# Optimization experiments

Measured on AMD Instinct MI355X. Metric: run time of the kernel, lower is better.

## Reference

```python
import jax, jax.numpy as jnp
import numpy as np

MASK_ID = 3
MAX_SEN = 128
SEN_DIM = 128
EMBED = 1024


def setup_inputs() -> dict:
    key = jax.random.key(0)
    ks = jax.random.split(key, 12)
    B, S, E, D = 8, 8192, EMBED, SEN_DIM
    s = 0.02
    return {
        "input_ids": jax.random.randint(ks[0], (B, S), 0, 64),
        "hidden_states": jax.random.normal(ks[1], (B, S, E), jnp.float32),
        "Wv": jax.random.normal(ks[2], (E, D), jnp.float32) * s,
        "bv": jnp.zeros((D,), jnp.float32),
        "Wq": jax.random.normal(ks[3], (E, D), jnp.float32) * s,
        "bq": jnp.zeros((D,), jnp.float32),
        "Wk": jax.random.normal(ks[4], (D, D), jnp.float32) * s,
        "bk": jnp.zeros((D,), jnp.float32),
        "Wvt": jax.random.normal(ks[5], (D, D), jnp.float32) * s,
        "bvt": jnp.zeros((D,), jnp.float32),
        "Wo": jax.random.normal(ks[6], (D, E), jnp.float32) * s,
        "bo": jnp.zeros((E,), jnp.float32),
    }


def reference(input_ids, hidden_states, Wv, bv, Wq, bq, Wk, bk, Wvt, bvt, Wo, bo):
    B, S, E = hidden_states.shape
    dt = hidden_states.dtype

    # sentence segmentation: each mask token t with running count c belongs to bucket c-1
    mask = input_ids == MASK_ID                               # (B, S)
    csum = jnp.cumsum(mask.astype(jnp.int32), axis=1)         # (B, S)
    # tokens that are not mask tokens (or overflow max_sen_num) go to dummy bucket MAX_SEN
    seg = jnp.where(mask & (csum <= MAX_SEN), csum - 1, MAX_SEN)  # (B, S)

    # segment-sum replacement for torch.bmm(sen_pos_mask, hidden_states)
    b_idx = jnp.arange(B)[:, None]
    pooled = jnp.zeros((B, MAX_SEN + 1, E), dt).at[b_idx, seg].add(hidden_states)[:, :MAX_SEN]  # (B, M, E)

    static_sen_states = pooled @ Wv + bv                      # (B, M, 128)

    q_token = (hidden_states @ Wq + bq) * (SEN_DIM ** -0.5)   # (B, S, 128)
    k_sen = static_sen_states @ Wk + bk                       # (B, M, 128)
    v_sen = static_sen_states @ Wvt + bvt                     # (B, M, 128)

    # token t may attend to sentences 0..csum[t]-1
    tmp_mask = (jnp.arange(MAX_SEN)[None, None, :] + 1) <= csum[:, :, None]  # (B, S, M)
    neg = jnp.finfo(dt).min
    logits = jnp.einsum('bsd,bmd->bsm', q_token, k_sen) + jnp.where(tmp_mask, jnp.zeros((), dt), neg)
    attn = jax.nn.softmax(logits, axis=-1) * tmp_mask.astype(dt)  # (B, S, M)

    sen_attn_output = jnp.einsum('bsm,bmd->bsd', attn, v_sen) @ Wo + bo  # (B, S, E)
    return sen_attn_output
```

## Files before the change

kernel.cpp:

```cpp
#include <hip/hip_runtime.h>
#include <hip/hip_bf16.h>

#define MASK_ID 3
#define MAX_SEN 128
#define NB 8
#define SEQ 8192
#define EMB 1024
#define DIM 128

typedef __attribute__((ext_vector_type(8))) short short8v;
typedef __attribute__((ext_vector_type(4))) float f32x4;

#define MFMA(a, b, c) __builtin_amdgcn_mfma_f32_16x16x32_bf16(a, b, c, 0, 0, 0)

__device__ __forceinline__ short f2b(float x) {
    union { float f; unsigned u; } v; v.f = x;
    unsigned r = (v.u + 0x7FFFu + ((v.u >> 16) & 1u)) >> 16;
    return (short)r;
}

__device__ __forceinline__ unsigned cvtpk(float a, float b) {
    unsigned r;
    asm("v_cvt_pk_bf16_f32 %0, %1, %2" : "=v"(r) : "v"(a), "v"(b));
    return r;
}

__global__ __launch_bounds__(1024) void seg_kernel(const int* __restrict__ ids,
                                                   int* __restrict__ pos,
                                                   int* __restrict__ nvis) {
    int b = blockIdx.x;
    int tid = threadIdx.x;
    __shared__ int sc[1024];
    __shared__ int sc2[1024];
    const int PER = SEQ / 1024;
    int base = b * SEQ + tid * PER;

    int ids_l[PER];
    int cnt = 0;
    #pragma unroll
    for (int j = 0; j < PER; j++) {
        ids_l[j] = ids[base + j];
        cnt += (ids_l[j] == MASK_ID) ? 1 : 0;
    }
    if (tid < MAX_SEN) pos[b * MAX_SEN + tid] = -1;
    sc[tid] = cnt;
    __syncthreads();

    int* src = sc;
    int* dst = sc2;
    for (int off = 1; off < 1024; off <<= 1) {
        int v = src[tid];
        if (tid >= off) v += src[tid - off];
        dst[tid] = v;
        __syncthreads();
        int* t = src; src = dst; dst = t;
    }
    int incl = src[tid];
    int run = incl - cnt;

    #pragma unroll
    for (int j = 0; j < PER; j++) {
        if (ids_l[j] == MASK_ID) {
            run++;
            if (run <= MAX_SEN) pos[b * MAX_SEN + run - 1] = tid * PER + j;
        }
        int nv = run; if (nv > MAX_SEN) nv = MAX_SEN;
        nvis[base + j] = nv;
    }
}

__global__ __launch_bounds__(256) void prep_w(const float* __restrict__ Wq,
                                              const float* __restrict__ Wo,
                                              short* __restrict__ WqTt,
                                              short* __restrict__ WoTt) {
    int t = blockIdx.x * 256 + threadIdx.x;
    {
        int fid = t >> 6, lp = t & 63;
        int c = fid >> 4, ks = (fid >> 3) & 1, cf = fid & 7;
        int e0 = c * 64 + ks * 32 + (lp >> 4) * 8;
        int d = cf * 16 + (lp & 15);
        short8v v;
        #pragma unroll
        for (int j = 0; j < 8; j++) v[j] = f2b(Wq[(size_t)(e0 + j) * 128 + d]);
        *(short8v*)(WqTt + fid * 512 + lp * 8) = v;
    }
    {
        int fid = t >> 6, lp = t & 63;
        int ef = fid >> 2, kk = fid & 3;
        int e = ef * 16 + (lp & 15);
        int dd0 = kk * 32 + (lp >> 4) * 8;
        short8v v;
        #pragma unroll
        for (int j = 0; j < 8; j++) v[j] = f2b(Wo[(size_t)(dd0 + j) * 1024 + e]);
        *(short8v*)(WoTt + fid * 512 + lp * 8) = v;
    }
}

__global__ __launch_bounds__(128) void statkv_kernel(const float* __restrict__ hidden,
                                                     const float* __restrict__ Wv, const float* __restrict__ bv,
                                                     const float* __restrict__ Wk, const float* __restrict__ bk,
                                                     const float* __restrict__ Wvt, const float* __restrict__ bvt,
                                                     const int* __restrict__ pos,
                                                     short* __restrict__ k_t, short* __restrict__ vT_t) {
    int mg = blockIdx.x;
    int b  = blockIdx.y;
    int d  = threadIdx.x;
    __shared__ float h[4][1024];
    __shared__ float st[4][128];
    int m0 = mg * 4;

    #pragma unroll
    for (int j = 0; j < 4; j++) {
        int p = pos[b * MAX_SEN + m0 + j];
        const float* hp = hidden + ((size_t)b * SEQ + (p < 0 ? 0 : p)) * EMB;
        #pragma unroll
        for (int ii = 0; ii < 2; ii++) {
            float4 v = {0.f, 0.f, 0.f, 0.f};
            if (p >= 0) v = *(const float4*)(hp + ii * 512 + d * 4);
            *(float4*)&h[j][ii * 512 + d * 4] = v;
        }
    }
    __syncthreads();

    float a0 = 0.f, a1 = 0.f, a2 = 0.f, a3 = 0.f;
    for (int e = 0; e < 1024; e += 4) {
        float w0 = Wv[(size_t)e * 128 + d];
        float w1 = Wv[(size_t)(e + 1) * 128 + d];
        float w2 = Wv[(size_t)(e + 2) * 128 + d];
        float w3 = Wv[(size_t)(e + 3) * 128 + d];
        float4 h0 = *(const float4*)&h[0][e];
        float4 h1 = *(const float4*)&h[1][e];
        float4 h2 = *(const float4*)&h[2][e];
        float4 h3 = *(const float4*)&h[3][e];
        a0 += h0.x * w0 + h0.y * w1 + h0.z * w2 + h0.w * w3;
        a1 += h1.x * w0 + h1.y * w1 + h1.z * w2 + h1.w * w3;
        a2 += h2.x * w0 + h2.y * w1 + h2.z * w2 + h2.w * w3;
        a3 += h3.x * w0 + h3.y * w1 + h3.z * w2 + h3.w * w3;
    }
    float bvd = bv[d];
    st[0][d] = bvd + a0;
    st[1][d] = bvd + a1;
    st[2][d] = bvd + a2;
    st[3][d] = bvd + a3;
    __syncthreads();

    float k0 = 0.f, k1 = 0.f, k2 = 0.f, k3 = 0.f;
    float v0 = 0.f, v1 = 0.f, v2 = 0.f, v3 = 0.f;
    for (int e = 0; e < 128; e += 4) {
        float wk0 = Wk[(e) * 128 + d],     wk1 = Wk[(e + 1) * 128 + d];
        float wk2 = Wk[(e + 2) * 128 + d], wk3 = Wk[(e + 3) * 128 + d];
        float wv0 = Wvt[(e) * 128 + d],     wv1 = Wvt[(e + 1) * 128 + d];
        float wv2 = Wvt[(e + 2) * 128 + d], wv3 = Wvt[(e + 3) * 128 + d];
        float4 s0 = *(const float4*)&st[0][e];
        float4 s1 = *(const float4*)&st[1][e];
        float4 s2 = *(const float4*)&st[2][e];
        float4 s3 = *(const float4*)&st[3][e];
        k0 += s0.x * wk0 + s0.y * wk1 + s0.z * wk2 + s0.w * wk3;
        k1 += s1.x * wk0 + s1.y * wk1 + s1.z * wk2 + s1.w * wk3;
        k2 += s2.x * wk0 + s2.y * wk1 + s2.z * wk2 + s2.w * wk3;
        k3 += s3.x * wk0 + s3.y * wk1 + s3.z * wk2 + s3.w * wk3;
        v0 += s0.x * wv0 + s0.y * wv1 + s0.z * wv2 + s0.w * wv3;
        v1 += s1.x * wv0 + s1.y * wv1 + s1.z * wv2 + s1.w * wv3;
        v2 += s2.x * wv0 + s2.y * wv1 + s2.z * wv2 + s2.w * wv3;
        v3 += s3.x * wv0 + s3.y * wv1 + s3.z * wv2 + s3.w * wv3;
    }
    float kv[4] = {k0, k1, k2, k3};
    float vv[4] = {v0, v1, v2, v3};
    float bkd = bk[d], bvtd = bvt[d];
    #pragma unroll
    for (int j = 0; j < 4; j++) {
        int m = m0 + j;
        int kk = d >> 5, lq = (d >> 3) & 3, jj = d & 7;
        int fid = (m >> 4) * 4 + kk;
        k_t[(b << 14) + fid * 512 + (lq * 16 + (m & 15)) * 8 + jj] = f2b(bkd + kv[j]);
        int df = d >> 4, kk2 = m >> 5, lq2 = (m >> 3) & 3, j2 = m & 7;
        int fid2 = df * 4 + kk2;
        vT_t[(b << 14) + fid2 * 512 + (lq2 * 16 + (d & 15)) * 8 + j2] = f2b(bvtd + vv[j]);
    }
}

__global__ __launch_bounds__(256, 3) void attn_kernel(
    const float* __restrict__ hidden,
    const short* __restrict__ WqTt, const float* __restrict__ bq,
    const short* __restrict__ k_t, const short* __restrict__ vT_t,
    const short* __restrict__ WoTt, const float* __restrict__ bo,
    const int* __restrict__ nvis,
    float* __restrict__ out) {
    int wg = (blockIdx.x & 7) * 128 + (blockIdx.x >> 3);
    int b  = wg >> 7;
    int s0 = (wg & 127) * 64;
    int tid = threadIdx.x;
    int lane = tid & 63;
    int w  = tid >> 6;
    int lr = lane & 15;
    int lq = lane >> 4;

    __shared__ __align__(16) char SH[49152];
    char* Ab  = SH;
    char* pPc = SH;
    char* odc = SH + 16384;
    char* qPc = SH + 32768;

    const size_t hrow = (size_t)b * SEQ + s0;
    f32x4 zero = {0.f, 0.f, 0.f, 0.f};

    f32x4 acc[4][2];
    #pragma unroll
    for (int rf = 0; rf < 4; rf++) { acc[rf][0] = zero; acc[rf][1] = zero; }

    int rsub = tid >> 4;
    int cfl  = (tid & 15) * 4;
    const float* hA0 = hidden + (hrow + 0 * 16 + rsub) * EMB + cfl;
    const float* hA1 = hidden + (hrow + 1 * 16 + rsub) * EMB + cfl;
    const float* hA2 = hidden + (hrow + 2 * 16 + rsub) * EMB + cfl;
    const float* hA3 = hidden + (hrow + 3 * 16 + rsub) * EMB + cfl;
    int swzA = (rsub & 7) << 4;
    int dA0 = (0 * 16 + rsub) * 128 + (((tid & 15) * 8) ^ swzA);
    int dA1 = (1 * 16 + rsub) * 128 + (((tid & 15) * 8) ^ swzA);
    int dA2 = (2 * 16 + rsub) * 128 + (((tid & 15) * 8) ^ swzA);
    int dA3 = (3 * 16 + rsub) * 128 + (((tid & 15) * 8) ^ swzA);

    float4 pa0[4], pa1[4], pa2[4];
    short8v W0[4], W1[4], W2[4];

#define LOADA(C, PA) do { \
    PA[0] = *(const float4*)(hA0 + (C) * 64); \
    PA[1] = *(const float4*)(hA1 + (C) * 64); \
    PA[2] = *(const float4*)(hA2 + (C) * 64); \
    PA[3] = *(const float4*)(hA3 + (C) * 64); } while (0)

#define LOADW(C, W) do { \
    const short* wp = WqTt + ((C) * 16 + 2 * w) * 512 + lane * 8; \
    W[0] = *(const short8v*)(wp); \
    W[1] = *(const short8v*)(wp + 512); \
    W[2] = *(const short8v*)(wp + 8 * 512); \
    W[3] = *(const short8v*)(wp + 9 * 512); } while (0)

#define STORE_A(PA) do { \
    unsigned long long v0_ = (unsigned long long)cvtpk(PA[0].z, PA[0].w) << 32 | cvtpk(PA[0].x, PA[0].y); \
    unsigned long long v1_ = (unsigned long long)cvtpk(PA[1].z, PA[1].w) << 32 | cvtpk(PA[1].x, PA[1].y); \
    unsigned long long v2_ = (unsigned long long)cvtpk(PA[2].z, PA[2].w) << 32 | cvtpk(PA[2].x, PA[2].y); \
    unsigned long long v3_ = (unsigned long long)cvtpk(PA[3].z, PA[3].w) << 32 | cvtpk(PA[3].x, PA[3].y); \
    *(unsigned long long*)(Ab + dA0) = v0_; \
    *(unsigned long long*)(Ab + dA1) = v1_; \
    *(unsigned long long*)(Ab + dA2) = v2_; \
    *(unsigned long long*)(Ab + dA3) = v3_; } while (0)

#define COMPUTE(W) do { \
    _Pragma("unroll") \
    for (int ks = 0; ks < 2; ks++) { \
        _Pragma("unroll") \
        for (int rf = 0; rf < 4; rf++) { \
            int row = rf * 16 + lr; \
            short8v fa = *(short8v*)(Ab + ((row * 128 + ks * 64 + lq * 16) ^ ((row & 7) << 4))); \
            acc[rf][0] = MFMA(fa, W[ks * 2 + 0], acc[rf][0]); \
            acc[rf][1] = MFMA(fa, W[ks * 2 + 1], acc[rf][1]); \
        } } } while (0)

#define ITER(c, PA, WW, DO_A, DO_W) do { \
    __builtin_amdgcn_s_barrier();                  \
    STORE_A(PA);                                   \
    if (DO_A) LOADA((c) + 3, PA); \
    asm volatile("s_waitcnt lgkmcnt(0)" ::: "memory"); \
    __builtin_amdgcn_sched_barrier(0); \
    __builtin_amdgcn_s_barrier();                  \
    COMPUTE(WW);                                   \
    if (DO_W) LOADW((c) + 3, WW);                  \
    } while (0)

    LOADA(0, pa0); LOADW(0, W0);
    LOADA(1, pa1); LOADW(1, W1);
    LOADA(2, pa2); LOADW(2, W2);

    ITER(0,  pa0, W0, 1, 1);
    ITER(1,  pa1, W1, 1, 1);
    ITER(2,  pa2, W2, 1, 1);
    ITER(3,  pa0, W0, 1, 1);
    ITER(4,  pa1, W1, 1, 1);
    ITER(5,  pa2, W2, 1, 1);
    ITER(6,  pa0, W0, 1, 1);
    ITER(7,  pa1, W1, 1, 1);
    ITER(8,  pa2, W2, 1, 1);
    ITER(9,  pa0, W0, 1, 1);
    ITER(10, pa1, W1, 1, 1);
    ITER(11, pa2, W2, 1, 1);
    ITER(12, pa0, W0, 1, 1);
    ITER(13, pa1, W1, 0, 0);
    ITER(14, pa2, W2, 0, 0);
    ITER(15, pa0, W0, 0, 0);

    {
        const float scale = 0.08838834764831845f;
        int d0 = w * 32 + lr;
        float bq0 = bq[d0], bq1 = bq[d0 + 16];
        #pragma unroll
        for (int rf = 0; rf < 4; rf++)
            #pragma unroll
            for (int r = 0; r < 4; r++) {
                int row = rf * 16 + lq * 4 + r;
                int x = (row & 7) << 4;
                *(short*)(qPc + row * 256 + ((d0 * 2) ^ x))        = f2b((acc[rf][0][r] + bq0) * scale);
                *(short*)(qPc + row * 256 + (((d0 + 16) * 2) ^ x)) = f2b((acc[rf][1][r] + bq1) * scale);
            }
    }
    __syncthreads();

    {
        f32x4 l[4][2];
        #pragma unroll
        for (int rf = 0; rf < 4; rf++) { l[rf][0] = zero; l[rf][1] = zero; }
        const short* kbase = k_t + (b << 14) + (2 * w) * 4 * 512 + lane * 8;
        #pragma unroll
        for (int kk = 0; kk < 4; kk++) {
            const short8v fb0 = *(const short8v*)(kbase + kk * 512);
            const short8v fb1 = *(const short8v*)(kbase + (4 + kk) * 512);
            #pragma unroll
            for (int rf = 0; rf < 4; rf++) {
                int row = rf * 16 + lr;
                int x = (row & 7) << 4;
                short8v fa = *(short8v*)(qPc + row * 256 + ((kk * 64 + lq * 16) ^ x));
                l[rf][0] = MFMA(fa, fb0, l[rf][0]);
                l[rf][1] = MFMA(fa, fb1, l[rf][1]);
            }
        }
        #pragma unroll
        for (int rf = 0; rf < 4; rf++)
            #pragma unroll
            for (int r = 0; r < 4; r++) {
                int row = rf * 16 + lq * 4 + r;
                int x = (row & 7) << 4;
                *(float*)(SH + row * 512 + (((w * 32 + lr) * 4) ^ x))      = l[rf][0][r];
                *(float*)(SH + row * 512 + (((w * 32 + 16 + lr) * 4) ^ x)) = l[rf][1][r];
            }
    }
    __syncthreads();

    {
        int t = tid >> 2, sub = tid & 3;
        int nv = nvis[b * SEQ + s0 + t];
        int x = (t & 7) << 4;
        float pv[32];
        #pragma unroll
        for (int u = 0; u < 8; u++) {
            float4 v = *(const float4*)(SH + t * 512 + ((sub * 128 + u * 16) ^ x));
            pv[u * 4]     = v.x; pv[u * 4 + 1] = v.y;
            pv[u * 4 + 2] = v.z; pv[u * 4 + 3] = v.w;
        }
        int base_m = sub * 32;
        float mx = -3.0e38f;
        #pragma unroll
        for (int i = 0; i < 32; i++)
            mx = (base_m + i < nv) ? fmaxf(mx, pv[i]) : mx;
        mx = fmaxf(mx, __shfl_xor(mx, 1));
        mx = fmaxf(mx, __shfl_xor(mx, 2));
        float sum = 0.f;
        #pragma unroll
        for (int i = 0; i < 32; i++) {
            float e = (base_m + i < nv) ? __expf(pv[i] - mx) : 0.f;
            pv[i] = e;
            sum += e;
        }
        sum += __shfl_xor(sum, 1);
        sum += __shfl_xor(sum, 2);
        float inv = (nv > 0) ? 1.0f / sum : 0.f;

        __syncthreads();

        #pragma unroll
        for (int u = 0; u < 4; u++) {
            union { short8v s; unsigned uu[4]; } p;
            #pragma unroll
            for (int i = 0; i < 4; i++)
                p.uu[i] = cvtpk(pv[u * 8 + 2 * i] * inv, pv[u * 8 + 2 * i + 1] * inv);
            *(short8v*)(pPc + t * 256 + ((sub * 64 + u * 16) ^ x)) = p.s;
        }
    }
    __syncthreads();

    {
        f32x4 o[4][2];
        #pragma unroll
        for (int rf = 0; rf < 4; rf++) { o[rf][0] = zero; o[rf][1] = zero; }
        const short* vbase = vT_t + (b << 14) + (2 * w) * 4 * 512 + lane * 8;
        #pragma unroll
        for (int kk = 0; kk < 4; kk++) {
            const short8v fb0 = *(const short8v*)(vbase + kk * 512);
            const short8v fb1 = *(const short8v*)(vbase + (4 + kk) * 512);
            #pragma unroll
            for (int rf = 0; rf < 4; rf++) {
                int row = rf * 16 + lr;
                int x = (row & 7) << 4;
                short8v fa = *(short8v*)(pPc + row * 256 + ((kk * 64 + lq * 16) ^ x));
                o[rf][0] = MFMA(fa, fb0, o[rf][0]);
                o[rf][1] = MFMA(fa, fb1, o[rf][1]);
            }
        }
        int d0 = w * 32 + lr;
        #pragma unroll
        for (int rf = 0; rf < 4; rf++)
            #pragma unroll
            for (int r = 0; r < 4; r++) {
                int row = rf * 16 + lq * 4 + r;
                int x = (row & 7) << 4;
                *(short*)(odc + row * 256 + ((d0 * 2) ^ x))        = f2b(o[rf][0][r]);
                *(short*)(odc + row * 256 + (((d0 + 16) * 2) ^ x)) = f2b(o[rf][1][r]);
            }
    }
    __syncthreads();

    {
        short8v af[4][4];
        #pragma unroll
        for (int rf = 0; rf < 4; rf++)
            #pragma unroll
            for (int kk = 0; kk < 4; kk++) {
                int row = rf * 16 + lr;
                int x = (row & 7) << 4;
                af[rf][kk] = *(short8v*)(odc + row * 256 + ((kk * 64 + lq * 16) ^ x));
            }
        #pragma unroll
        for (int grp = 0; grp < 4; grp++) {
            int colbase = w * 256 + grp * 64;
            f32x4 ac[4][4];
            #pragma unroll
            for (int rf = 0; rf < 4; rf++)
                #pragma unroll
                for (int cf = 0; cf < 4; cf++) ac[rf][cf] = zero;
            #pragma unroll
            for (int kk = 0; kk < 4; kk++) {
                #pragma unroll
                for (int cf = 0; cf < 4; cf++) {
                    const short8v bb = *(const short8v*)(WoTt
                        + ((w * 16 + grp * 4 + cf) * 4 + kk) * 512 + lane * 8);
                    #pragma unroll
                    for (int rf = 0; rf < 4; rf++)
                        ac[rf][cf] = MFMA(af[rf][kk], bb, ac[rf][cf]);
                }
            }
            #pragma unroll
            for (int cf = 0; cf < 4; cf++) {
                int col = colbase + cf * 16 + lr;
                float bov = bo[col];
                #pragma unroll
                for (int rf = 0; rf < 4; rf++)
                    #pragma unroll
                    for (int r = 0; r < 4; r++)
                        out[(hrow + rf * 16 + lq * 4 + r) * EMB + col] = ac[rf][cf][r] + bov;
            }
        }
    }
}

extern "C" void kernel_launch(void* const* d_in, const int* in_sizes, int n_in,
                              void* d_out, int out_size, void* d_ws, size_t ws_size,
                              hipStream_t stream) {
    const int*   ids    = (const int*)d_in[0];
    const float* hidden = (const float*)d_in[1];
    const float* Wv     = (const float*)d_in[2];
    const float* bv     = (const float*)d_in[3];
    const float* Wq     = (const float*)d_in[4];
    const float* bq     = (const float*)d_in[5];
    const float* Wk     = (const float*)d_in[6];
    const float* bk     = (const float*)d_in[7];
    const float* Wvt    = (const float*)d_in[8];
    const float* bvt    = (const float*)d_in[9];
    const float* Wo     = (const float*)d_in[10];
    const float* bo     = (const float*)d_in[11];

    char* ws = (char*)d_ws;
    int*   pos   = (int*)ws;
    int*   nvis  = (int*)(ws + (4 << 10));
    short* k_t   = (short*)(ws + (260 << 10));
    short* vT_t  = (short*)(ws + (516 << 10));
    short* WqTt  = (short*)(ws + (772 << 10));
    short* WoTt  = (short*)(ws + (1028 << 10));

    seg_kernel<<<NB, 1024, 0, stream>>>(ids, pos, nvis);
    prep_w<<<64, 256, 0, stream>>>(Wq, Wo, WqTt, WoTt);
    dim3 g2(32, NB);
    statkv_kernel<<<g2, 128, 0, stream>>>(hidden, Wv, bv, Wk, bk, Wvt, bvt, pos, k_t, vT_t);
    attn_kernel<<<NB * (SEQ / 64), 256, 0, stream>>>(hidden, WqTt, bq, k_t, vT_t, WoTt, bo,
                                                     nvis, (float*)d_out);
}
```

Baseline: 233.2 us.

## Stage output tiles through LDS for coalesced float4 stores; shrink W prefetch ring

The final Wo projection now writes each 16-row by 256-column accumulator tile into shared memory, then reads it back so every thread stores contiguous float4 chunks (bias added) to global memory. Before, each lane wrote scattered scalar floats, which wastes write bandwidth on a large fp32 output. The column assignment across warps changes so each group covers a contiguous 256-column block. Separately, the Wq weight prefetch ring drops from three buffers to two, cutting register use. The cost is extra barriers and LDS traffic per row fragment, plus a shallower weight prefetch.

```diff
diff --git a/kernel.cpp b/kernel.cpp
--- a/kernel.cpp
+++ b/kernel.cpp
@@ -221,7 +221,7 @@
     int dA3 = (3 * 16 + rsub) * 128 + (((tid & 15) * 8) ^ swzA);
 
     float4 pa0[4], pa1[4], pa2[4];
-    short8v W0[4], W1[4], W2[4];
+    short8v Wa[4], Wb[4];
 
 #define LOADA(C, PA) do { \
     PA[0] = *(const float4*)(hA0 + (C) * 64); \
@@ -265,29 +265,31 @@
     __builtin_amdgcn_sched_barrier(0); \
     __builtin_amdgcn_s_barrier();                  \
     COMPUTE(WW);                                   \
-    if (DO_W) LOADW((c) + 3, WW);                  \
+    if (DO_W) LOADW((c) + 2, WW);                  \
     } while (0)
 
-    LOADA(0, pa0); LOADW(0, W0);
-    LOADA(1, pa1); LOADW(1, W1);
-    LOADA(2, pa2); LOADW(2, W2);
-
-    ITER(0,  pa0, W0, 1, 1);
-    ITER(1,  pa1, W1, 1, 1);
-    ITER(2,  pa2, W2, 1, 1);
-    ITER(3,  pa0, W0, 1, 1);
-    ITER(4,  pa1, W1, 1, 1);
-    ITER(5,  pa2, W2, 1, 1);
-    ITER(6,  pa0, W0, 1, 1);
-    ITER(7,  pa1, W1, 1, 1);
-    ITER(8,  pa2, W2, 1, 1);
-    ITER(9,  pa0, W0, 1, 1);
-    ITER(10, pa1, W1, 1, 1);
-    ITER(11, pa2, W2, 1, 1);
-    ITER(12, pa0, W0, 1, 1);
-    ITER(13, pa1, W1, 0, 0);
-    ITER(14, pa2, W2, 0, 0);
-    ITER(15, pa0, W0, 0, 0);
+    LOADW(0, Wa);
+    LOADW(1, Wb);
+    LOADA(0, pa0);
+    LOADA(1, pa1);
+    LOADA(2, pa2);
+
+    ITER(0,  pa0, Wa, 1, 1);
+    ITER(1,  pa1, Wb, 1, 1);
+    ITER(2,  pa2, Wa, 1, 1);
+    ITER(3,  pa0, Wb, 1, 1);
+    ITER(4,  pa1, Wa, 1, 1);
+    ITER(5,  pa2, Wb, 1, 1);
+    ITER(6,  pa0, Wa, 1, 1);
+    ITER(7,  pa1, Wb, 1, 1);
+    ITER(8,  pa2, Wa, 1, 1);
+    ITER(9,  pa0, Wb, 1, 1);
+    ITER(10, pa1, Wa, 1, 1);
+    ITER(11, pa2, Wb, 1, 1);
+    ITER(12, pa0, Wa, 1, 1);
+    ITER(13, pa1, Wb, 0, 1);
+    ITER(14, pa2, Wa, 0, 0);
+    ITER(15, pa0, Wb, 0, 0);
 
     {
         const float scale = 0.08838834764831845f;
@@ -418,9 +420,14 @@
                 int x = (row & 7) << 4;
                 af[rf][kk] = *(short8v*)(odc + row * 256 + ((kk * 64 + lq * 16) ^ x));
             }
+        __syncthreads();
+
+        float* cst = (float*)SH;
+        int srow2 = tid >> 4;
+        int scidx = (tid & 15) * 4;
+
         #pragma unroll
         for (int grp = 0; grp < 4; grp++) {
-            int colbase = w * 256 + grp * 64;
             f32x4 ac[4][4];
             #pragma unroll
             for (int rf = 0; rf < 4; rf++)
@@ -431,21 +438,29 @@
                 #pragma unroll
                 for (int cf = 0; cf < 4; cf++) {
                     const short8v bb = *(const short8v*)(WoTt
-                        + ((w * 16 + grp * 4 + cf) * 4 + kk) * 512 + lane * 8);
+                        + ((grp * 16 + w * 4 + cf) * 4 + kk) * 512 + lane * 8);
                     #pragma unroll
                     for (int rf = 0; rf < 4; rf++)
                         ac[rf][cf] = MFMA(af[rf][kk], bb, ac[rf][cf]);
                 }
             }
             #pragma unroll
-            for (int cf = 0; cf < 4; cf++) {
-                int col = colbase + cf * 16 + lr;
-                float bov = bo[col];
+            for (int rf = 0; rf < 4; rf++) {
                 #pragma unroll
-                for (int rf = 0; rf < 4; rf++)
+                for (int cf = 0; cf < 4; cf++)
                     #pragma unroll
                     for (int r = 0; r < 4; r++)
-                        out[(hrow + rf * 16 + lq * 4 + r) * EMB + col] = ac[rf][cf][r] + bov;
+                        cst[(lq * 4 + r) * 260 + w * 64 + cf * 16 + lr] = ac[rf][cf][r];
+                __syncthreads();
+                #pragma unroll
+                for (int i = 0; i < 4; i++) {
+                    int cidx = scidx + i * 64;
+                    float4 v = *(const float4*)(cst + srow2 * 260 + cidx);
+                    float4 b4 = *(const float4*)(bo + grp * 256 + cidx);
+                    v.x += b4.x; v.y += b4.y; v.z += b4.z; v.w += b4.w;
+                    *(float4*)(&out[(hrow + rf * 16 + srow2) * EMB + grp * 256 + cidx]) = v;
+                }
+                __syncthreads();
             }
         }
     }
```

Measured after the change: 217.2 us. 6.8% less time.
